# Performance work log

Hardware: AMD Instinct MI355X
Metric: run time of the kernel (lower is better)

## Reference

```python
import jax, jax.numpy as jnp
import numpy as np

THETA = 10000.0
B, S, D, H = 2, 2048, 1024, 16
DK = D // H


def setup_inputs() -> dict:
    key = jax.random.key(0)
    k1, k2, k3 = jax.random.split(key, 3)
    x = jax.random.normal(k1, (B, S, D), jnp.float32)
    # trunc_normal init approximated by scaled normal (std = 2/(d_k+d_model))
    weight = jax.random.normal(k2, (3, H, DK, D), jnp.float32) * (2.0 / (DK + D))
    wo_weight = jax.random.normal(k3, (D, H * DK), jnp.float32) * (2.0 / (2 * D))
    token_positions = jnp.arange(S, dtype=jnp.int32)
    return {"x": x, "token_positions": token_positions, "weight": weight, "wo_weight": wo_weight}


def _rope(x, cos, sin):
    # x: (..., seq, d_k); rotate interleaved pairs
    x1 = jnp.stack((-x[..., 1::2], x[..., ::2]), axis=-1).reshape(x.shape)
    return x * cos + x1 * sin


def _masked_softmax(scores, mask):
    # matches reference: exp(x - rowmax over ALL entries), zero masked, normalize, zero again
    e = jnp.exp(scores - jnp.max(scores, axis=-1, keepdims=True))
    e = jnp.where(mask, e, 0.0)
    a = e / jnp.sum(e, axis=-1, keepdims=True)
    return jnp.where(mask, a, 0.0)


def reference(x, token_positions, weight, wo_weight):
    dk = weight.shape[2]
    seq_len = x.shape[-2]
    # fused QKV projection: (b, 3, h, s, dk)
    qkv = jnp.einsum('bsd,qhkd->bqhsk', x, weight)
    # RoPE tables from token positions
    pos = token_positions.astype(jnp.float32)[:, None]          # (s, 1)
    kidx = jnp.arange(1, dk // 2 + 1, dtype=jnp.float32)[None]  # (1, dk/2)
    theta = pos / (THETA ** ((2.0 * kidx - 2.0) / dk))          # (s, dk/2)
    cos = jnp.repeat(jnp.cos(theta), 2, axis=-1)                # (s, dk)
    sin = jnp.repeat(jnp.sin(theta), 2, axis=-1)
    q = _rope(qkv[:, 0], cos, sin)   # (b, h, s, dk)
    k = _rope(qkv[:, 1], cos, sin)
    v = qkv[:, 2]
    scores = jnp.einsum('bhqd,bhkd->bhqk', q, k) / jnp.sqrt(jnp.float32(dk))
    mask = jnp.tril(jnp.ones((seq_len, seq_len), dtype=bool))
    att = _masked_softmax(scores, mask)
    out = jnp.einsum('bhqk,bhkd->bhqd', att, v)                 # (b, h, s, dv)
    out = jnp.transpose(out, (0, 2, 1, 3)).reshape(*x.shape[:-1], -1)  # (b, s, h*dv)
    return jnp.einsum('bsi,oi->bso', out, wo_weight)
```

## Files before the change

kernel.cpp:

```cpp
#include <hip/hip_runtime.h>
#include <hip/hip_bf16.h>
#include <math.h>

#define B_   2
#define S_   2048
#define D_   1024
#define H_   16
#define DK_  64
#define NQKV 3072
#define M_   (B_ * S_)

typedef unsigned short u16;
typedef unsigned int   u32;
typedef __attribute__((ext_vector_type(8))) short short8;
typedef __attribute__((ext_vector_type(4))) float f32x4;
typedef __attribute__((ext_vector_type(4))) u16   u16x4;

typedef const __attribute__((address_space(1))) void* gvptr;
typedef __attribute__((address_space(3))) void* lvptr;

#define QSCALE 0.18033688011f

#if __has_builtin(__builtin_amdgcn_exp2f)
#define EXP2F(x) __builtin_amdgcn_exp2f(x)
#else
#define EXP2F(x) __expf(0.69314718056f * (x))
#endif

__device__ __forceinline__ u16 f2bf(float f) {
  union { float f; u32 u; } v; v.f = f;
  u32 r = v.u + 0x7FFF + ((v.u >> 16) & 1);
  return (u16)(r >> 16);
}
__device__ __forceinline__ float bf2f(u16 h) {
  union { u32 u; float f; } v; v.u = ((u32)h) << 16;
  return v.f;
}
__device__ __forceinline__ u32 cvtpk_bf16(float lo, float hi) {
  u32 r;
  asm("v_cvt_pk_bf16_f32 %0, %1, %2" : "=v"(r) : "v"(lo), "v"(hi));
  return r;
}

#define MEMFENCE() asm volatile("" ::: "memory")
#define RAW_BARRIER() do { MEMFENCE(); __builtin_amdgcn_s_barrier(); MEMFENCE(); } while (0)

#define SWZ(r) ((((r) & 7) ^ ((((r) >> 3) & 1) << 2)))

__global__ void rope_cs_kernel(const int* __restrict__ pos,
                               float2* __restrict__ cs) {
  int idx = blockIdx.x * 256 + threadIdx.x;
  int i = idx & 31;
  int s = idx >> 5;
  double p = (double)pos[s];
  double t = p * pow(10000.0, -(double)i / 32.0);
  cs[idx] = make_float2((float)cos(t), (float)sin(t));
}

#define N4X (M_ * D_ / 4)
#define N4W (NQKV * D_ / 4)
#define N4WO (D_ * D_ / 4)
__global__ void cvt_all_kernel(const float* __restrict__ x,
                               const float* __restrict__ w,
                               const float* __restrict__ wo,
                               u16* __restrict__ dst) {
  int i = blockIdx.x * 256 + threadIdx.x;
  float4 v;
  if (i < N4X)            v = ((const float4*)x)[i];
  else if (i < N4X + N4W) v = ((const float4*)w)[i - N4X];
  else                    v = ((const float4*)wo)[i - (N4X + N4W)];
  u16x4 o;
  o[0] = f2bf(v.x); o[1] = f2bf(v.y); o[2] = f2bf(v.z); o[3] = f2bf(v.w);
  ((u16x4*)dst)[i] = o;
}

template<bool OUT_BF16, bool ROPE>
__global__ __launch_bounds__(256) void gemm_nt_mfma(const u16* __restrict__ A,
                                                    const u16* __restrict__ Bm,
                                                    void* __restrict__ Cout,
                                                    const float2* __restrict__ cstab,
                                                    int Nd, int Kd) {
  __shared__ u16 As[2][128 * 64];
  __shared__ u16 Bs[2][128 * 64];
  const int t  = threadIdx.x;
  const int w  = t >> 6, l = t & 63;
  const int g  = l >> 4, ln = l & 15;
  const int wm = w >> 1, wn = w & 1;
  const int m0 = blockIdx.y * 128, n0 = blockIdx.x * 128;

  const int sr = t >> 3;
  auto stage = [&](int buf, int k0) {
#pragma unroll
    for (int p = 0; p < 4; ++p) {
      int r = p * 32 + sr;
      int sx = (t & 7) ^ (r & 7);
      __builtin_amdgcn_global_load_lds(
          (gvptr)(A + (size_t)(m0 + r) * Kd + k0 + sx * 8),
          (lvptr)(&As[buf][(p * 256 + w * 64) * 8]), 16, 0, 0);
      __builtin_amdgcn_global_load_lds(
          (gvptr)(Bm + (size_t)(n0 + r) * Kd + k0 + sx * 8),
          (lvptr)(&Bs[buf][(p * 256 + w * 64) * 8]), 16, 0, 0);
    }
  };

  const f32x4 vzero = {0.f, 0.f, 0.f, 0.f};
  f32x4 acc[4][4];
#pragma unroll
  for (int i = 0; i < 4; ++i)
#pragma unroll
    for (int j = 0; j < 4; ++j) acc[i][j] = vzero;

  const int nkt = Kd >> 6;
  stage(0, 0);
  int cur = 0;
#pragma unroll 1
  for (int kt = 0; kt < nkt; ++kt) {
    if (kt + 1 < nkt) {
      stage(cur ^ 1, (kt + 1) * 64);
      asm volatile("s_waitcnt vmcnt(8)" ::: "memory");
    } else {
      asm volatile("s_waitcnt vmcnt(0)" ::: "memory");
    }
    RAW_BARRIER();

    __builtin_amdgcn_s_setprio(1);
#pragma unroll
    for (int ks = 0; ks < 2; ++ks) {
      short8 af[4], bf[4];
#pragma unroll
      for (int i = 0; i < 4; ++i) {
        int ra = wm * 64 + i * 16 + ln;
        af[i] = *(const short8*)&As[cur][ra * 64 + (((ks * 4 + g) ^ (ra & 7)) * 8)];
        int rb = wn * 64 + i * 16 + ln;
        bf[i] = *(const short8*)&Bs[cur][rb * 64 + (((ks * 4 + g) ^ (rb & 7)) * 8)];
      }
#pragma unroll
      for (int i = 0; i < 4; ++i)
#pragma unroll
        for (int j = 0; j < 4; ++j)
          acc[i][j] = __builtin_amdgcn_mfma_f32_16x16x32_bf16(af[i], bf[j], acc[i][j], 0, 0, 0);
    }
    __builtin_amdgcn_s_setprio(0);

    asm volatile("s_waitcnt lgkmcnt(0)" ::: "memory");
    RAW_BARRIER();
    cur ^= 1;
  }

  if (ROPE && n0 < 2048) {
#pragma unroll
    for (int i = 0; i < 4; ++i)
#pragma unroll
      for (int r = 0; r < 4; ++r) {
        int rowi = m0 + wm * 64 + i * 16 + g * 4 + r;
        int srow = rowi & (S_ - 1);
#pragma unroll
        for (int j = 0; j < 4; ++j) {
          int dk = j * 16 + ln;
          float2 cs = cstab[srow * 32 + (dk >> 1)];
          float v = acc[i][j][r];
          float p = __shfl_xor(v, 1);
          float sn = (ln & 1) ? cs.y : -cs.y;
          float rot = fmaf(p, sn, v * cs.x);
          ((u16*)Cout)[(size_t)rowi * Nd + n0 + wn * 64 + j * 16 + ln] = f2bf(rot);
        }
      }
  } else {
#pragma unroll
    for (int i = 0; i < 4; ++i)
#pragma unroll
      for (int j = 0; j < 4; ++j)
#pragma unroll
        for (int r = 0; r < 4; ++r) {
          size_t row = (size_t)(m0 + wm * 64 + i * 16 + g * 4 + r);
          size_t col = (size_t)(n0 + wn * 64 + j * 16 + ln);
          if (OUT_BF16) ((u16*)Cout)[row * Nd + col] = f2bf(acc[i][j][r]);
          else          ((float*)Cout)[row * Nd + col] = acc[i][j][r];
        }
  }
}

__global__ __launch_bounds__(256) void v_transpose_kernel(const u16* __restrict__ qkvb,
                                                          u16* __restrict__ Vt) {
  __shared__ u16 tile[64][72];
  const int t = threadIdx.x;
  const int s0 = blockIdx.x * 64, h = blockIdx.y, b = blockIdx.z;
  {
    int r = t >> 2, cs = (t & 3) * 16;
    const u16* src = qkvb + (size_t)(b * S_ + s0 + r) * NQKV + 2048 + h * 64 + cs;
    u16 v[16];
    *(uint4*)&v[0] = *(const uint4*)src;
    *(uint4*)&v[8] = *(const uint4*)(src + 8);
#pragma unroll
    for (int j = 0; j < 16; ++j) tile[cs + j][r] = v[j];
  }
  __syncthreads();
  {
    int d = t >> 2, ss = (t & 3) * 16;
    u16 o[16];
#pragma unroll
    for (int j = 0; j < 16; ++j) o[j] = tile[d][ss + j];
    u16* dst = Vt + ((size_t)(b * H_ + h) * 64 + d) * S_ + s0 + ss;
    *(uint4*)&dst[0] = *(uint4*)&o[0];
    *(uint4*)&dst[8] = *(uint4*)&o[8];
  }
}

__global__ __launch_bounds__(512) void attn_mfma(const u16* __restrict__ qkvb,
                                                 const u16* __restrict__ Vt,
                                                 u16* __restrict__ attb) {
  __shared__ u16 Ks[3][64 * 64];
  __shared__ u16 Vs[3][64 * 64];
  const int t = threadIdx.x;
  const int w = t >> 6, l = t & 63;
  const int g = l >> 4, ln = l & 15;
  const int h = blockIdx.y, b = blockIdx.z;
  const size_t bS = (size_t)b * S_;
  const u16* Kbase = qkvb + bS * NQKV + D_ + h * 64;
  const u16* Vbase = Vt + (size_t)(b * H_ + h) * 64 * S_;

  const int sr = t >> 3;
  const int ssx = (t & 7) ^ SWZ(sr);
  auto stage = [&](int buf, int k0) {
    __builtin_amdgcn_global_load_lds(
        (gvptr)(Kbase + (size_t)(k0 + sr) * NQKV + ssx * 8),
        (lvptr)(&Ks[buf][w * 512]), 16, 0, 0);
    __builtin_amdgcn_global_load_lds(
        (gvptr)(Vbase + (size_t)sr * S_ + k0 + ssx * 8),
        (lvptr)(&Vs[buf][w * 512]), 16, 0, 0);
  };

  const f32x4 vzero = {0.f, 0.f, 0.f, 0.f};

#pragma unroll 1
  for (int half = 0; half < 2; ++half) {
    const int tq = (half == 0) ? (15 - blockIdx.x) : blockIdx.x;
    const int q0 = tq * 128;
    const int nt = 2 * tq + 2;
    const int qg = q0 + w * 16 + ln;
    const int wqmax = q0 + w * 16 + 15;

    short8 qf[2];
    {
      const u16* qrow = qkvb + (bS + q0 + w * 16 + ln) * NQKV + h * 64;
      qf[0] = *(const short8*)(qrow + g * 8);
      qf[1] = *(const short8*)(qrow + 32 + g * 8);
#pragma unroll
      for (int kx = 0; kx < 2; ++kx)
#pragma unroll
        for (int e = 0; e < 8; ++e)
          qf[kx][e] = (short)f2bf(bf2f((u16)qf[kx][e]) * QSCALE);
    }

    f32x4 o[4];
#pragma unroll
    for (int dt = 0; dt < 4; ++dt) o[dt] = vzero;
    float mrun = -INFINITY, lrun = 0.f;

    stage(0, 0);
    stage(1, 64);
    int cur = 0;

#pragma unroll 1
    for (int kt = 0; kt < nt; ++kt) {
      const int k0 = kt * 64;
      if (kt + 2 < nt) {
        int pre = cur + 2; if (pre >= 3) pre -= 3;
        stage(pre, k0 + 128);
        asm volatile("s_waitcnt vmcnt(4)" ::: "memory");
      } else if (kt + 1 < nt) {
        asm volatile("s_waitcnt vmcnt(2)" ::: "memory");
      } else {
        asm volatile("s_waitcnt vmcnt(0)" ::: "memory");
      }
      RAW_BARRIER();

      if (k0 <= wqmax) {
        f32x4 sacc[4];
#pragma unroll
        for (int st = 0; st < 4; ++st) sacc[st] = vzero;
        __builtin_amdgcn_s_setprio(1);
#pragma unroll
        for (int st = 0; st < 4; ++st) {
          const int pr = ((ln >> 2) << 3) + ((st & 1) << 2) + (ln & 3) + ((st >> 1) << 5);
#pragma unroll
          for (int ks = 0; ks < 2; ++ks) {
            short8 kf = *(const short8*)&Ks[cur][pr * 64 + (((ks * 4 + g) ^ SWZ(pr)) * 8)];
            sacc[st] = __builtin_amdgcn_mfma_f32_16x16x32_bf16(kf, qf[ks], sacc[st], 0, 0, 0);
          }
        }
        __builtin_amdgcn_s_setprio(0);

        float tmax = -INFINITY;
        if (k0 + 63 > q0 + w * 16) {
#pragma unroll
          for (int st = 0; st < 4; ++st)
#pragma unroll
            for (int r = 0; r < 4; ++r) {
              int key = k0 + g * 8 + ((st & 1) << 2) + r + ((st >> 1) << 5);
              if (key > qg) sacc[st][r] = -INFINITY;
              tmax = fmaxf(tmax, sacc[st][r]);
            }
        } else {
#pragma unroll
          for (int st = 0; st < 4; ++st)
#pragma unroll
            for (int r = 0; r < 4; ++r) tmax = fmaxf(tmax, sacc[st][r]);
        }
        tmax = fmaxf(tmax, __shfl_xor(tmax, 16));
        tmax = fmaxf(tmax, __shfl_xor(tmax, 32));
        float al = 1.f, mnew = mrun;
        if (!__all(tmax <= mrun + 8.0f)) {
          mnew = fmaxf(mrun, tmax);
          al = EXP2F(mrun - mnew);
#pragma unroll
          for (int r = 0; r < 4; ++r) {
            float srs = __shfl(al, g * 4 + r);
#pragma unroll
            for (int dt = 0; dt < 4; ++dt) o[dt][r] *= srs;
          }
        }
        float lsum = 0.f;
#pragma unroll
        for (int st = 0; st < 4; ++st)
#pragma unroll
          for (int r = 0; r < 4; ++r) {
            float pe = EXP2F(sacc[st][r] - mnew);
            sacc[st][r] = pe;
            lsum += pe;
          }
        lsum += __shfl_xor(lsum, 16);
        lsum += __shfl_xor(lsum, 32);
        lrun = lrun * al + lsum;
        mrun = mnew;

        union { u32 u[4]; short8 v; } pa[2];
        pa[0].u[0] = cvtpk_bf16(sacc[0][0], sacc[0][1]);
        pa[0].u[1] = cvtpk_bf16(sacc[0][2], sacc[0][3]);
        pa[0].u[2] = cvtpk_bf16(sacc[1][0], sacc[1][1]);
        pa[0].u[3] = cvtpk_bf16(sacc[1][2], sacc[1][3]);
        pa[1].u[0] = cvtpk_bf16(sacc[2][0], sacc[2][1]);
        pa[1].u[1] = cvtpk_bf16(sacc[2][2], sacc[2][3]);
        pa[1].u[2] = cvtpk_bf16(sacc[3][0], sacc[3][1]);
        pa[1].u[3] = cvtpk_bf16(sacc[3][2], sacc[3][3]);

        __builtin_amdgcn_s_setprio(1);
#pragma unroll
        for (int ks = 0; ks < 2; ++ks)
#pragma unroll
          for (int dt = 0; dt < 4; ++dt) {
            const int dr = dt * 16 + ln;
            short8 vf = *(const short8*)&Vs[cur][dr * 64 + (((ks * 4 + g) ^ SWZ(dr)) * 8)];
            o[dt] = __builtin_amdgcn_mfma_f32_16x16x32_bf16(pa[ks].v, vf, o[dt], 0, 0, 0);
          }
        __builtin_amdgcn_s_setprio(0);
      }

      asm volatile("s_waitcnt lgkmcnt(0)" ::: "memory");
      RAW_BARRIER();
      cur = (cur == 2) ? 0 : cur + 1;
    }

    float linv = 1.f / lrun;
#pragma unroll
    for (int r = 0; r < 4; ++r) {
      float ir = __shfl(linv, g * 4 + r);
      size_t row = bS + q0 + w * 16 + g * 4 + r;
#pragma unroll
      for (int dt = 0; dt < 4; ++dt)
        attb[row * D_ + h * 64 + dt * 16 + ln] = f2bf(o[dt][r] * ir);
    }
    asm volatile("s_waitcnt vmcnt(0)" ::: "memory");
  }
}

extern "C" void kernel_launch(void* const* d_in, const int* in_sizes, int n_in,
                              void* d_out, int out_size, void* d_ws, size_t ws_size,
                              hipStream_t stream) {
  (void)in_sizes; (void)n_in; (void)out_size; (void)ws_size;
  const float* x   = (const float*)d_in[0];
  const int*   pos = (const int*)d_in[1];
  const float* w   = (const float*)d_in[2];
  const float* wo  = (const float*)d_in[3];
  float* out = (float*)d_out;

  u16* qkvb = (u16*)d_ws;
  u16* Vt   = qkvb + (size_t)M_ * NQKV;
  u16* attb = Vt + (size_t)B_ * H_ * 64 * S_;
  u16* xb   = attb + (size_t)M_ * D_;
  u16* wb   = xb + (size_t)M_ * D_;
  u16* wob  = wb + (size_t)NQKV * D_;
  float2* cstab = (float2*)(wob + (size_t)D_ * D_);

  rope_cs_kernel<<<(S_ * 32) / 256, 256, 0, stream>>>(pos, cstab);

  cvt_all_kernel<<<(N4X + N4W + N4WO) / 256, 256, 0, stream>>>(x, w, wo, xb);

  gemm_nt_mfma<true, true><<<dim3(NQKV / 128, M_ / 128), 256, 0, stream>>>(
      xb, wb, qkvb, cstab, NQKV, D_);

  v_transpose_kernel<<<dim3(S_ / 64, H_, B_), 256, 0, stream>>>(qkvb, Vt);

  attn_mfma<<<dim3(8, H_, B_), 512, 0, stream>>>(qkvb, Vt, attb);

  gemm_nt_mfma<false, false><<<dim3(D_ / 128, M_ / 128), 256, 0, stream>>>(
      attb, wob, out, nullptr, D_, D_);
}
```

Measured before the change: 203.2 us.

## Share K/V tiles across paired query blocks and use smaller output GEMM tiles

```diff
diff --git a/kernel.cpp b/kernel.cpp
--- a/kernel.cpp
+++ b/kernel.cpp
@@ -180,6 +180,87 @@
   }
 }
 
+__global__ __launch_bounds__(256) void gemm_small_mfma(const u16* __restrict__ A,
+                                                       const u16* __restrict__ Bm,
+                                                       float* __restrict__ C,
+                                                       int Nd, int Kd) {
+  __shared__ u16 As[2][64 * 64];
+  __shared__ u16 Bs[2][64 * 64];
+  const int t  = threadIdx.x;
+  const int w  = t >> 6, l = t & 63;
+  const int g  = l >> 4, ln = l & 15;
+  const int wm = w >> 1, wn = w & 1;
+  const int m0 = blockIdx.y * 64, n0 = blockIdx.x * 64;
+
+  auto stage = [&](int buf, int k0) {
+#pragma unroll
+    for (int p = 0; p < 2; ++p) {
+      int c = p * 256 + t;
+      int r = c >> 3;
+      int sx = (c & 7) ^ (r & 7);
+      __builtin_amdgcn_global_load_lds(
+          (gvptr)(A + (size_t)(m0 + r) * Kd + k0 + sx * 8),
+          (lvptr)(&As[buf][(p * 256 + w * 64) * 8]), 16, 0, 0);
+      __builtin_amdgcn_global_load_lds(
+          (gvptr)(Bm + (size_t)(n0 + r) * Kd + k0 + sx * 8),
+          (lvptr)(&Bs[buf][(p * 256 + w * 64) * 8]), 16, 0, 0);
+    }
+  };
+
+  const f32x4 vzero = {0.f, 0.f, 0.f, 0.f};
+  f32x4 acc[2][2];
+#pragma unroll
+  for (int i = 0; i < 2; ++i)
+#pragma unroll
+    for (int j = 0; j < 2; ++j) acc[i][j] = vzero;
+
+  const int nkt = Kd >> 6;
+  stage(0, 0);
+  int cur = 0;
+#pragma unroll 1
+  for (int kt = 0; kt < nkt; ++kt) {
+    if (kt + 1 < nkt) {
+      stage(cur ^ 1, (kt + 1) * 64);
+      asm volatile("s_waitcnt vmcnt(4)" ::: "memory");
+    } else {
+      asm volatile("s_waitcnt vmcnt(0)" ::: "memory");
+    }
+    RAW_BARRIER();
+
+    __builtin_amdgcn_s_setprio(1);
+#pragma unroll
+    for (int ks = 0; ks < 2; ++ks) {
+      short8 af[2], bf[2];
+#pragma unroll
+      for (int i = 0; i < 2; ++i) {
+        int ra = wm * 32 + i * 16 + ln;
+        af[i] = *(const short8*)&As[cur][ra * 64 + (((ks * 4 + g) ^ (ra & 7)) * 8)];
+        int rb = wn * 32 + i * 16 + ln;
+        bf[i] = *(const short8*)&Bs[cur][rb * 64 + (((ks * 4 + g) ^ (rb & 7)) * 8)];
+      }
+#pragma unroll
+      for (int i = 0; i < 2; ++i)
+#pragma unroll
+        for (int j = 0; j < 2; ++j)
+          acc[i][j] = __builtin_amdgcn_mfma_f32_16x16x32_bf16(af[i], bf[j], acc[i][j], 0, 0, 0);
+    }
+    __builtin_amdgcn_s_setprio(0);
+
+    asm volatile("s_waitcnt lgkmcnt(0)" ::: "memory");
+    RAW_BARRIER();
+    cur ^= 1;
+  }
+
+#pragma unroll
+  for (int i = 0; i < 2; ++i)
+#pragma unroll
+    for (int j = 0; j < 2; ++j)
+#pragma unroll
+      for (int r = 0; r < 4; ++r)
+        C[(size_t)(m0 + wm * 32 + i * 16 + g * 4 + r) * Nd + n0 + wn * 32 + j * 16 + ln]
+            = acc[i][j][r];
+}
+
 __global__ __launch_bounds__(256) void v_transpose_kernel(const u16* __restrict__ qkvb,
                                                           u16* __restrict__ Vt) {
   __shared__ u16 tile[64][72];
@@ -209,168 +290,187 @@
 __global__ __launch_bounds__(512) void attn_mfma(const u16* __restrict__ qkvb,
                                                  const u16* __restrict__ Vt,
                                                  u16* __restrict__ attb) {
-  __shared__ u16 Ks[3][64 * 64];
-  __shared__ u16 Vs[3][64 * 64];
+  __shared__ u16 Ks[2][128 * 64];
+  __shared__ u16 Vs[2][64 * 128];
   const int t = threadIdx.x;
   const int w = t >> 6, l = t & 63;
   const int g = l >> 4, ln = l & 15;
-  const int h = blockIdx.y, b = blockIdx.z;
+  const int bx = blockIdx.x, h = blockIdx.y, b = blockIdx.z;
   const size_t bS = (size_t)b * S_;
   const u16* Kbase = qkvb + bS * NQKV + D_ + h * 64;
   const u16* Vbase = Vt + (size_t)(b * H_ + h) * 64 * S_;
 
-  const int sr = t >> 3;
-  const int ssx = (t & 7) ^ SWZ(sr);
   auto stage = [&](int buf, int k0) {
-    __builtin_amdgcn_global_load_lds(
-        (gvptr)(Kbase + (size_t)(k0 + sr) * NQKV + ssx * 8),
-        (lvptr)(&Ks[buf][w * 512]), 16, 0, 0);
-    __builtin_amdgcn_global_load_lds(
-        (gvptr)(Vbase + (size_t)sr * S_ + k0 + ssx * 8),
-        (lvptr)(&Vs[buf][w * 512]), 16, 0, 0);
+#pragma unroll
+    for (int p = 0; p < 2; ++p) {
+      int ck = p * 512 + t;
+      int rk = ck >> 3, sk = (ck & 7) ^ SWZ(rk);
+      __builtin_amdgcn_global_load_lds(
+          (gvptr)(Kbase + (size_t)(k0 + rk) * NQKV + sk * 8),
+          (lvptr)(&Ks[buf][(p * 512 + w * 64) * 8]), 16, 0, 0);
+      int cv = p * 512 + t;
+      int rv = cv >> 4, sv = (cv & 15) ^ (rv & 15);
+      __builtin_amdgcn_global_load_lds(
+          (gvptr)(Vbase + (size_t)rv * S_ + k0 + sv * 8),
+          (lvptr)(&Vs[buf][(p * 512 + w * 64) * 8]), 16, 0, 0);
+    }
   };
 
   const f32x4 vzero = {0.f, 0.f, 0.f, 0.f};
 
+  const int tqH = 15 - bx, tqL = bx;
+  const int q0H = tqH * 128, q0L = tqL * 128;
+  const int nt = 16 - bx;
+  const int ntL = bx + 1;
+  const int qgH = q0H + w * 16 + ln;
+  const int qgL = q0L + w * 16 + ln;
+
+  short8 qfH[2], qfL[2];
+  {
+    const u16* qr = qkvb + (bS + q0H + w * 16 + ln) * NQKV + h * 64;
+    qfH[0] = *(const short8*)(qr + g * 8);
+    qfH[1] = *(const short8*)(qr + 32 + g * 8);
+    qr = qkvb + (bS + q0L + w * 16 + ln) * NQKV + h * 64;
+    qfL[0] = *(const short8*)(qr + g * 8);
+    qfL[1] = *(const short8*)(qr + 32 + g * 8);
+#pragma unroll
+    for (int kx = 0; kx < 2; ++kx)
+#pragma unroll
+      for (int e = 0; e < 8; ++e) {
+        qfH[kx][e] = (short)f2bf(bf2f((u16)qfH[kx][e]) * QSCALE);
+        qfL[kx][e] = (short)f2bf(bf2f((u16)qfL[kx][e]) * QSCALE);
+      }
+  }
+
+  f32x4 oH[4], oL[4];
+#pragma unroll
+  for (int dt = 0; dt < 4; ++dt) { oH[dt] = vzero; oL[dt] = vzero; }
+  float mH = -INFINITY, lH = 0.f, mL = -INFINITY, lL = 0.f;
+
+  auto chain = [&](const short8* qf, f32x4* o, float& mrun, float& lrun,
+                   int qg, bool maskTile, int k0, int cur) {
+    f32x4 sacc[8];
+#pragma unroll
+    for (int st = 0; st < 8; ++st) sacc[st] = vzero;
+    __builtin_amdgcn_s_setprio(1);
+#pragma unroll
+    for (int st = 0; st < 8; ++st) {
+      const int pr = ((ln >> 2) << 3) + ((st & 1) << 2) + (ln & 3) + ((st >> 1) << 5);
+#pragma unroll
+      for (int ks = 0; ks < 2; ++ks) {
+        short8 kf = *(const short8*)&Ks[cur][pr * 64 + (((ks * 4 + g) ^ SWZ(pr)) * 8)];
+        sacc[st] = __builtin_amdgcn_mfma_f32_16x16x32_bf16(kf, qf[ks], sacc[st], 0, 0, 0);
+      }
+    }
+    __builtin_amdgcn_s_setprio(0);
+
+    float tmax = -INFINITY;
+    if (maskTile) {
+#pragma unroll
+      for (int st = 0; st < 8; ++st)
+#pragma unroll
+        for (int r = 0; r < 4; ++r) {
+          int key = k0 + g * 8 + ((st & 1) << 2) + r + ((st >> 1) << 5);
+          if (key > qg) sacc[st][r] = -INFINITY;
+          tmax = fmaxf(tmax, sacc[st][r]);
+        }
+    } else {
+#pragma unroll
+      for (int st = 0; st < 8; ++st)
+#pragma unroll
+        for (int r = 0; r < 4; ++r) tmax = fmaxf(tmax, sacc[st][r]);
+    }
+    tmax = fmaxf(tmax, __shfl_xor(tmax, 16));
+    tmax = fmaxf(tmax, __shfl_xor(tmax, 32));
+    float al = 1.f, mnew = mrun;
+    if (!__all(tmax <= mrun + 8.0f)) {
+      mnew = fmaxf(mrun, tmax);
+      al = EXP2F(mrun - mnew);
+#pragma unroll
+      for (int r = 0; r < 4; ++r) {
+        float srs = __shfl(al, g * 4 + r);
+#pragma unroll
+        for (int dt = 0; dt < 4; ++dt) o[dt][r] *= srs;
+      }
+    }
+    float lsum = 0.f;
+#pragma unroll
+    for (int st = 0; st < 8; ++st)
+#pragma unroll
+      for (int r = 0; r < 4; ++r) {
+        float pe = EXP2F(sacc[st][r] - mnew);
+        sacc[st][r] = pe;
+        lsum += pe;
+      }
+    lsum += __shfl_xor(lsum, 16);
+    lsum += __shfl_xor(lsum, 32);
+    lrun = lrun * al + lsum;
+    mrun = mnew;
+
+    union { u32 u[4]; short8 v; } pa[4];
+#pragma unroll
+    for (int ks = 0; ks < 4; ++ks) {
+      pa[ks].u[0] = cvtpk_bf16(sacc[2 * ks][0], sacc[2 * ks][1]);
+      pa[ks].u[1] = cvtpk_bf16(sacc[2 * ks][2], sacc[2 * ks][3]);
+      pa[ks].u[2] = cvtpk_bf16(sacc[2 * ks + 1][0], sacc[2 * ks + 1][1]);
+      pa[ks].u[3] = cvtpk_bf16(sacc[2 * ks + 1][2], sacc[2 * ks + 1][3]);
+    }
+
+    __builtin_amdgcn_s_setprio(1);
+#pragma unroll
+    for (int ks = 0; ks < 4; ++ks)
+#pragma unroll
+      for (int dt = 0; dt < 4; ++dt) {
+        const int dr = dt * 16 + ln;
+        short8 vf = *(const short8*)&Vs[cur][dr * 128 + (((ks * 4 + g) ^ (dr & 15)) * 8)];
+        o[dt] = __builtin_amdgcn_mfma_f32_16x16x32_bf16(pa[ks].v, vf, o[dt], 0, 0, 0);
+      }
+    __builtin_amdgcn_s_setprio(0);
+  };
+
+  stage(0, 0);
+  int cur = 0;
 #pragma unroll 1
-  for (int half = 0; half < 2; ++half) {
-    const int tq = (half == 0) ? (15 - blockIdx.x) : blockIdx.x;
-    const int q0 = tq * 128;
-    const int nt = 2 * tq + 2;
-    const int qg = q0 + w * 16 + ln;
-    const int wqmax = q0 + w * 16 + 15;
-
-    short8 qf[2];
-    {
-      const u16* qrow = qkvb + (bS + q0 + w * 16 + ln) * NQKV + h * 64;
-      qf[0] = *(const short8*)(qrow + g * 8);
-      qf[1] = *(const short8*)(qrow + 32 + g * 8);
-#pragma unroll
-      for (int kx = 0; kx < 2; ++kx)
-#pragma unroll
-        for (int e = 0; e < 8; ++e)
-          qf[kx][e] = (short)f2bf(bf2f((u16)qf[kx][e]) * QSCALE);
-    }
-
-    f32x4 o[4];
-#pragma unroll
-    for (int dt = 0; dt < 4; ++dt) o[dt] = vzero;
-    float mrun = -INFINITY, lrun = 0.f;
-
-    stage(0, 0);
-    stage(1, 64);
-    int cur = 0;
-
-#pragma unroll 1
-    for (int kt = 0; kt < nt; ++kt) {
-      const int k0 = kt * 64;
-      if (kt + 2 < nt) {
-        int pre = cur + 2; if (pre >= 3) pre -= 3;
-        stage(pre, k0 + 128);
-        asm volatile("s_waitcnt vmcnt(4)" ::: "memory");
-      } else if (kt + 1 < nt) {
-        asm volatile("s_waitcnt vmcnt(2)" ::: "memory");
-      } else {
-        asm volatile("s_waitcnt vmcnt(0)" ::: "memory");
-      }
-      RAW_BARRIER();
-
-      if (k0 <= wqmax) {
-        f32x4 sacc[4];
-#pragma unroll
-        for (int st = 0; st < 4; ++st) sacc[st] = vzero;
-        __builtin_amdgcn_s_setprio(1);
-#pragma unroll
-        for (int st = 0; st < 4; ++st) {
-          const int pr = ((ln >> 2) << 3) + ((st & 1) << 2) + (ln & 3) + ((st >> 1) << 5);
-#pragma unroll
-          for (int ks = 0; ks < 2; ++ks) {
-            short8 kf = *(const short8*)&Ks[cur][pr * 64 + (((ks * 4 + g) ^ SWZ(pr)) * 8)];
-            sacc[st] = __builtin_amdgcn_mfma_f32_16x16x32_bf16(kf, qf[ks], sacc[st], 0, 0, 0);
-          }
-        }
-        __builtin_amdgcn_s_setprio(0);
-
-        float tmax = -INFINITY;
-        if (k0 + 63 > q0 + w * 16) {
-#pragma unroll
-          for (int st = 0; st < 4; ++st)
-#pragma unroll
-            for (int r = 0; r < 4; ++r) {
-              int key = k0 + g * 8 + ((st & 1) << 2) + r + ((st >> 1) << 5);
-              if (key > qg) sacc[st][r] = -INFINITY;
-              tmax = fmaxf(tmax, sacc[st][r]);
-            }
-        } else {
-#pragma unroll
-          for (int st = 0; st < 4; ++st)
-#pragma unroll
-            for (int r = 0; r < 4; ++r) tmax = fmaxf(tmax, sacc[st][r]);
-        }
-        tmax = fmaxf(tmax, __shfl_xor(tmax, 16));
-        tmax = fmaxf(tmax, __shfl_xor(tmax, 32));
-        float al = 1.f, mnew = mrun;
-        if (!__all(tmax <= mrun + 8.0f)) {
-          mnew = fmaxf(mrun, tmax);
-          al = EXP2F(mrun - mnew);
-#pragma unroll
-          for (int r = 0; r < 4; ++r) {
-            float srs = __shfl(al, g * 4 + r);
-#pragma unroll
-            for (int dt = 0; dt < 4; ++dt) o[dt][r] *= srs;
-          }
-        }
-        float lsum = 0.f;
-#pragma unroll
-        for (int st = 0; st < 4; ++st)
-#pragma unroll
-          for (int r = 0; r < 4; ++r) {
-            float pe = EXP2F(sacc[st][r] - mnew);
-            sacc[st][r] = pe;
-            lsum += pe;
-          }
-        lsum += __shfl_xor(lsum, 16);
-        lsum += __shfl_xor(lsum, 32);
-        lrun = lrun * al + lsum;
-        mrun = mnew;
-
-        union { u32 u[4]; short8 v; } pa[2];
-        pa[0].u[0] = cvtpk_bf16(sacc[0][0], sacc[0][1]);
-        pa[0].u[1] = cvtpk_bf16(sacc[0][2], sacc[0][3]);
-        pa[0].u[2] = cvtpk_bf16(sacc[1][0], sacc[1][1]);
-        pa[0].u[3] = cvtpk_bf16(sacc[1][2], sacc[1][3]);
-        pa[1].u[0] = cvtpk_bf16(sacc[2][0], sacc[2][1]);
-        pa[1].u[1] = cvtpk_bf16(sacc[2][2], sacc[2][3]);
-        pa[1].u[2] = cvtpk_bf16(sacc[3][0], sacc[3][1]);
-        pa[1].u[3] = cvtpk_bf16(sacc[3][2], sacc[3][3]);
-
-        __builtin_amdgcn_s_setprio(1);
-#pragma unroll
-        for (int ks = 0; ks < 2; ++ks)
-#pragma unroll
-          for (int dt = 0; dt < 4; ++dt) {
-            const int dr = dt * 16 + ln;
-            short8 vf = *(const short8*)&Vs[cur][dr * 64 + (((ks * 4 + g) ^ SWZ(dr)) * 8)];
-            o[dt] = __builtin_amdgcn_mfma_f32_16x16x32_bf16(pa[ks].v, vf, o[dt], 0, 0, 0);
-          }
-        __builtin_amdgcn_s_setprio(0);
-      }
-
-      asm volatile("s_waitcnt lgkmcnt(0)" ::: "memory");
-      RAW_BARRIER();
-      cur = (cur == 2) ? 0 : cur + 1;
-    }
-
-    float linv = 1.f / lrun;
+  for (int kt = 0; kt < nt; ++kt) {
+    const int k0 = kt * 128;
+    if (kt + 1 < nt) {
+      stage(cur ^ 1, k0 + 128);
+      asm volatile("s_waitcnt vmcnt(4)" ::: "memory");
+    } else {
+      asm volatile("s_waitcnt vmcnt(0)" ::: "memory");
+    }
+    RAW_BARRIER();
+
+    chain(qfH, oH, mH, lH, qgH, kt == nt - 1, k0, cur);
+    if (kt < ntL)
+      chain(qfL, oL, mL, lL, qgL, kt == tqL, k0, cur);
+
+    asm volatile("s_waitcnt lgkmcnt(0)" ::: "memory");
+    RAW_BARRIER();
+    cur ^= 1;
+  }
+
+  {
+    float linv = 1.f / lH;
 #pragma unroll
     for (int r = 0; r < 4; ++r) {
       float ir = __shfl(linv, g * 4 + r);
-      size_t row = bS + q0 + w * 16 + g * 4 + r;
+      size_t row = bS + q0H + w * 16 + g * 4 + r;
 #pragma unroll
       for (int dt = 0; dt < 4; ++dt)
-        attb[row * D_ + h * 64 + dt * 16 + ln] = f2bf(o[dt][r] * ir);
-    }
-    asm volatile("s_waitcnt vmcnt(0)" ::: "memory");
+        attb[row * D_ + h * 64 + dt * 16 + ln] = f2bf(oH[dt][r] * ir);
+    }
+  }
+  {
+    float linv = 1.f / lL;
+#pragma unroll
+    for (int r = 0; r < 4; ++r) {
+      float ir = __shfl(linv, g * 4 + r);
+      size_t row = bS + q0L + w * 16 + g * 4 + r;
+#pragma unroll
+      for (int dt = 0; dt < 4; ++dt)
+        attb[row * D_ + h * 64 + dt * 16 + ln] = f2bf(oL[dt][r] * ir);
+    }
   }
 }
 
@@ -403,6 +503,6 @@
 
   attn_mfma<<<dim3(8, H_, B_), 512, 0, stream>>>(qkvb, Vt, attb);
 
-  gemm_nt_mfma<false, false><<<dim3(D_ / 128, M_ / 128), 256, 0, stream>>>(
-      attb, wob, out, nullptr, D_, D_);
-}
+  gemm_small_mfma<<<dim3(D_ / 64, M_ / 64), 256, 0, stream>>>(
+      attb, wob, out, D_, D_);
+}
```

After: 189.3 us. -6.8%, faster.
